# Kernel tuning notes

Measured on AMD Instinct MI355X. Metric: run time of the kernel, lower is better.

The kernel has to match this reference:

```python
import jax, jax.numpy as jnp
import numpy as np
from jax import lax

SEQ, BATCH, IN, HID, OUT = 28, 8192, 28, 128, 10


def _lstm_layer(x, W_ih, W_hh, b_ih, b_hh):
    # x: [T, B, in]; PyTorch gate order: i, f, g, o
    # precompute input projection once (keeps scan body memory-bound on h only)
    xproj = jnp.einsum('tbi,gi->tbg', x, W_ih) + b_ih + b_hh  # [T, B, 4H]
    H = W_hh.shape[1]
    B = x.shape[1]
    h0 = jnp.zeros((B, H), x.dtype)
    c0 = jnp.zeros((B, H), x.dtype)

    def step(carry, xp_t):
        h, c = carry
        gates = xp_t + h @ W_hh.T  # [B, 4H]
        i, f, g, o = jnp.split(gates, 4, axis=-1)
        i = jax.nn.sigmoid(i)
        f = jax.nn.sigmoid(f)
        g = jnp.tanh(g)
        o = jax.nn.sigmoid(o)
        c = f * c + i * g
        h = o * jnp.tanh(c)
        return (h, c), h

    _, ys = lax.scan(step, (h0, c0), xproj)
    return ys  # [T, B, H]


def setup_inputs() -> dict:
    key = jax.random.key(0)
    ks = jax.random.split(key, 11)
    s_in = 1.0 / np.sqrt(HID)
    u = lambda k, shape: jax.random.uniform(k, shape, jnp.float32, -s_in, s_in)
    return {
        'X': jax.random.normal(ks[0], (SEQ, BATCH, IN), jnp.float32),
        'W_ih0': u(ks[1], (4 * HID, IN)),
        'W_hh0': u(ks[2], (4 * HID, HID)),
        'b_ih0': u(ks[3], (4 * HID,)),
        'b_hh0': u(ks[4], (4 * HID,)),
        'W_ih1': u(ks[5], (4 * HID, HID)),
        'W_hh1': u(ks[6], (4 * HID, HID)),
        'b_ih1': u(ks[7], (4 * HID,)),
        'b_hh1': u(ks[8], (4 * HID,)),
        'W_lin': u(ks[9], (OUT, HID)),
        'b_lin': u(ks[10], (OUT,)),
    }


def reference(X, W_ih0, W_hh0, b_ih0, b_hh0, W_ih1, W_hh1, b_ih1, b_hh1, W_lin, b_lin):
    h1 = _lstm_layer(X, W_ih0, W_hh0, b_ih0, b_hh0)   # [T, B, 128]
    h2 = _lstm_layer(h1, W_ih1, W_hh1, b_ih1, b_hh1)  # [T, B, 128]
    pred = h2[-1] @ W_lin.T + b_lin                   # [B, 10]
    return pred
```

## Files before the change

kernel.cpp:

```cpp
#include <hip/hip_runtime.h>
#include <hip/hip_bf16.h>

#define SEQ   28
#define BATCH 8192
#define NIN   28
#define HID   128
#define NOUT  10

#define SCL_SIG  (-1.4426950408889634f)
#define SCL_TANH (2.8853900817779268f)

typedef __bf16 bf16_t;
typedef __bf16 bf16x8 __attribute__((ext_vector_type(8)));
typedef float  f32x4  __attribute__((ext_vector_type(4)));

__device__ __forceinline__ unsigned swz(unsigned row, unsigned byte_in_row) {
    return row * 256u + (byte_in_row ^ ((row & 7u) << 4));
}
__device__ __forceinline__ float clamp40(float x) {
    return fminf(fmaxf(x, -40.0f), 40.0f);
}

__global__ void pack_all_kernel(const float* __restrict__ X,    bf16_t* __restrict__ xpk,
                                const float* __restrict__ Whh0, bf16_t* __restrict__ whhp0,
                                const float* __restrict__ Whh1, bf16_t* __restrict__ whhp1,
                                const float* __restrict__ Wih1, bf16_t* __restrict__ wihp1) {
    const int XN = SEQ * BATCH * 32;
    const int WN = 512 * 128;
    const int total = XN + 3 * WN;
    for (int idx = blockIdx.x * blockDim.x + threadIdx.x; idx < total;
         idx += gridDim.x * blockDim.x) {
        if (idx < XN) {
            int k  = idx & 31;
            int tb = idx >> 5;
            float v = (k < NIN) ? X[(size_t)tb * NIN + k] : 0.0f;
            xpk[idx] = (bf16_t)v;
        } else {
            int r  = idx - XN;
            int mi = r / WN, e = r - mi * WN;
            const float* W = (mi == 0) ? Whh0 : (mi == 1) ? Whh1 : Wih1;
            bf16_t*      o = (mi == 0) ? whhp0 : (mi == 1) ? whhp1 : wihp1;
            int j    = e & 7;
            int frag = e >> 3;
            int lane = frag & 63;
            int ksnt = frag >> 6;
            int nt = ksnt & 31, ks = ksnt >> 5;
            int gate = nt * 16 + (lane & 15);
            int k    = ks * 32 + ((lane >> 4) << 3) + j;
            float s  = ((gate >> 7) == 2) ? SCL_TANH : SCL_SIG;
            o[e] = (bf16_t)(W[gate * 128 + k] * s);
        }
    }
}

template <int LAYER>
__global__ __launch_bounds__(512, 2)
void lstm_kernel(const float* __restrict__ Wih,
                 const float* __restrict__ bih,
                 const float* __restrict__ bhh,
                 const bf16_t* __restrict__ xin,
                 const bf16_t* __restrict__ whhp,
                 const bf16_t* __restrict__ wihp,
                 bf16_t* __restrict__ h1out,
                 const float* __restrict__ Wlin,
                 const float* __restrict__ blin,
                 float* __restrict__ out)
{
    constexpr int KS   = (LAYER == 0) ? 1 : 4;
    constexpr int XSTR = (LAYER == 0) ? 32 : 128;

    __shared__ unsigned char smem[16384] __attribute__((aligned(16)));

    const int tid  = threadIdx.x;
    const int lane = tid & 63;
    const int w    = tid >> 6;
    const int l15  = lane & 15;
    const int l4   = lane >> 4;
    const int rb   = blockIdx.x * 32;

    for (int i = tid * 16; i < 16384; i += 512 * 16) {
        f32x4 z = {0.f, 0.f, 0.f, 0.f};
        *(f32x4*)(smem + i) = z;
    }

    float bias[4];
    #pragma unroll
    for (int q = 0; q < 4; ++q) {
        int col = 16 * w + 128 * q + l15;
        float s = (q == 2) ? SCL_TANH : SCL_SIG;
        bias[q] = (bih[col] + bhh[col]) * s;
    }

    bf16x8 whh[4][4];
    #pragma unroll
    for (int q = 0; q < 4; ++q)
        #pragma unroll
        for (int ks = 0; ks < 4; ++ks)
            whh[q][ks] = *(const bf16x8*)(whhp + ((size_t)((ks * 32 + (w + 8 * q)) * 64 + lane)) * 8);

    bf16x8 wih1[4][4];
    bf16x8 wih0[4];
    if (LAYER == 1) {
        #pragma unroll
        for (int q = 0; q < 4; ++q)
            #pragma unroll
            for (int ks = 0; ks < 4; ++ks)
                wih1[q][ks] = *(const bf16x8*)(wihp + ((size_t)((ks * 32 + (w + 8 * q)) * 64 + lane)) * 8);
    } else {
        #pragma unroll
        for (int q = 0; q < 4; ++q) {
            int gate = 16 * w + 128 * q + l15;
            float s = (q == 2) ? SCL_TANH : SCL_SIG;
            #pragma unroll
            for (int j = 0; j < 8; ++j) {
                int k = l4 * 8 + j;
                wih0[q][j] = (k < NIN) ? (bf16_t)(Wih[gate * NIN + k] * s) : (bf16_t)0.0f;
            }
        }
    }

    float c[2][4] = {};

    bf16x8 x[KS][2];
    #pragma unroll
    for (int ks = 0; ks < KS; ++ks)
        #pragma unroll
        for (int m = 0; m < 2; ++m)
            x[ks][m] = *(const bf16x8*)(xin + (size_t)(rb + 16 * m + l15) * XSTR + ks * 32 + l4 * 8);

    __syncthreads();

    for (int t = 0; t < SEQ; ++t) {
        unsigned char* hb = smem + ((t & 1) << 13);
        unsigned char* hn = smem + ((~t & 1) << 13);

        bf16x8 ah[4][2];
        #pragma unroll
        for (int ks = 0; ks < 4; ++ks)
            #pragma unroll
            for (int m = 0; m < 2; ++m)
                ah[ks][m] = *(const bf16x8*)(hb + swz(16 * m + l15, (ks * 32 + l4 * 8) * 2));

        f32x4 acc[2][4];
        #pragma unroll
        for (int m = 0; m < 2; ++m)
            #pragma unroll
            for (int q = 0; q < 4; ++q) {
                f32x4 b = {bias[q], bias[q], bias[q], bias[q]};
                acc[m][q] = b;
            }

        #pragma unroll
        for (int m = 0; m < 2; ++m)
            #pragma unroll
            for (int q = 0; q < 4; ++q)
                #pragma unroll
                for (int ks = 0; ks < KS; ++ks)
                    acc[m][q] = __builtin_amdgcn_mfma_f32_16x16x32_bf16(
                        x[ks][m], (LAYER == 1) ? wih1[q][ks] : wih0[q], acc[m][q], 0, 0, 0);

        if (t + 1 < SEQ) {
            #pragma unroll
            for (int ks = 0; ks < KS; ++ks)
                #pragma unroll
                for (int m = 0; m < 2; ++m)
                    x[ks][m] = *(const bf16x8*)(xin + (size_t)((t + 1) * BATCH + rb + 16 * m + l15) * XSTR + ks * 32 + l4 * 8);
        }

        #pragma unroll
        for (int m = 0; m < 2; ++m)
            #pragma unroll
            for (int q = 0; q < 4; ++q)
                #pragma unroll
                for (int ks = 0; ks < 4; ++ks)
                    acc[m][q] = __builtin_amdgcn_mfma_f32_16x16x32_bf16(
                        ah[ks][m], whh[q][ks], acc[m][q], 0, 0, 0);

        #pragma unroll
        for (int m = 0; m < 2; ++m)
            #pragma unroll
            for (int r = 0; r < 4; ++r) {
                float Ei = __builtin_amdgcn_exp2f(clamp40(acc[m][0][r]));
                float Ef = __builtin_amdgcn_exp2f(clamp40(acc[m][1][r]));
                float Eg = __builtin_amdgcn_exp2f(clamp40(acc[m][2][r]));
                float Eo = __builtin_amdgcn_exp2f(clamp40(acc[m][3][r]));
                float ti = 1.0f + Ei, tf = 1.0f + Ef;
                float tg = 1.0f + Eg, to = 1.0f + Eo;
                float gt = 1.0f - 2.0f * __builtin_amdgcn_rcpf(tg);
                float num = fmaf(c[m][r], ti, gt * tf);
                float cn  = num * __builtin_amdgcn_rcpf(tf * ti);
                c[m][r] = cn;
                float Ec = __builtin_amdgcn_exp2f(clamp40(SCL_TANH * cn));
                float hv = (Ec - 1.0f) * __builtin_amdgcn_rcpf(to * (1.0f + Ec));
                *(bf16_t*)(hn + swz(16 * m + l4 * 4 + r, (16 * w + l15) * 2)) = (bf16_t)hv;
            }
        __syncthreads();

        if (LAYER == 0) {
            int row = tid >> 4, sc = tid & 15;
            f32x4 v = *(const f32x4*)(hn + swz(row, sc * 16));
            *(f32x4*)((unsigned char*)h1out + ((size_t)(t * BATCH + rb + row)) * 256 + sc * 16) = v;
        }
    }

    if (LAYER == 1) {
        if (tid < 32 * NOUT) {
            int row = tid / NOUT, oc = tid % NOUT;
            const unsigned char* hf = smem;
            float s = blin[oc];
            #pragma unroll 8
            for (int k = 0; k < HID; ++k) {
                float h = (float)*(const bf16_t*)(hf + swz(row, k * 2));
                s += h * Wlin[oc * HID + k];
            }
            out[(size_t)(rb + row) * NOUT + oc] = s;
        }
    }
}

extern "C" void kernel_launch(void* const* d_in, const int* in_sizes, int n_in,
                              void* d_out, int out_size, void* d_ws, size_t ws_size,
                              hipStream_t stream) {
    const float* X    = (const float*)d_in[0];
    const float* Wih0 = (const float*)d_in[1];
    const float* Whh0 = (const float*)d_in[2];
    const float* bih0 = (const float*)d_in[3];
    const float* bhh0 = (const float*)d_in[4];
    const float* Wih1 = (const float*)d_in[5];
    const float* Whh1 = (const float*)d_in[6];
    const float* bih1 = (const float*)d_in[7];
    const float* bhh1 = (const float*)d_in[8];
    const float* Wlin = (const float*)d_in[9];
    const float* blin = (const float*)d_in[10];
    float* out = (float*)d_out;

    unsigned char* ws = (unsigned char*)d_ws;
    bf16_t* xpk   = (bf16_t*)(ws);
    bf16_t* h1    = (bf16_t*)(ws + 14680064);
    bf16_t* whhp0 = (bf16_t*)(ws + 73400320);
    bf16_t* whhp1 = (bf16_t*)(ws + 73531392);
    bf16_t* wihp1 = (bf16_t*)(ws + 73662464);

    pack_all_kernel<<<dim3(4096), dim3(256), 0, stream>>>(
        X, xpk, Whh0, whhp0, Whh1, whhp1, Wih1, wihp1);

    lstm_kernel<0><<<dim3(256), dim3(512), 0, stream>>>(
        Wih0, bih0, bhh0, xpk, whhp0, (const bf16_t*)nullptr, h1,
        (const float*)nullptr, (const float*)nullptr, (float*)nullptr);

    lstm_kernel<1><<<dim3(256), dim3(512), 0, stream>>>(
        (const float*)nullptr, bih1, bhh1, h1, whhp1, wihp1, (bf16_t*)nullptr,
        Wlin, blin, out);
}
```

Measured before the change: 138.5 us.

## Fuse both LSTM layers into one kernel and convert X on the fly

Both LSTM layers now run in a single kernel: each block processes its 32 batch rows through layer 0, then reloads layer-1 weights and runs layer 1 on the h1 values it just wrote. The separate bf16 packing pass over X is removed; layer 0 reads fp32 X directly and converts it in registers. The clamps before exp2 in the gate math are also dropped. This saves a kernel launch, a large intermediate write and read, and some ALU work per step. The trade-off is a small risk of inf/NaN for extreme pre-activations, plus a longer single kernel.

```diff
diff --git a/kernel.cpp b/kernel.cpp
--- a/kernel.cpp
+++ b/kernel.cpp
@@ -17,58 +17,134 @@
 __device__ __forceinline__ unsigned swz(unsigned row, unsigned byte_in_row) {
     return row * 256u + (byte_in_row ^ ((row & 7u) << 4));
 }
-__device__ __forceinline__ float clamp40(float x) {
-    return fminf(fmaxf(x, -40.0f), 40.0f);
-}
-
-__global__ void pack_all_kernel(const float* __restrict__ X,    bf16_t* __restrict__ xpk,
-                                const float* __restrict__ Whh0, bf16_t* __restrict__ whhp0,
-                                const float* __restrict__ Whh1, bf16_t* __restrict__ whhp1,
-                                const float* __restrict__ Wih1, bf16_t* __restrict__ wihp1) {
-    const int XN = SEQ * BATCH * 32;
-    const int WN = 512 * 128;
-    const int total = XN + 3 * WN;
-    for (int idx = blockIdx.x * blockDim.x + threadIdx.x; idx < total;
-         idx += gridDim.x * blockDim.x) {
-        if (idx < XN) {
-            int k  = idx & 31;
-            int tb = idx >> 5;
-            float v = (k < NIN) ? X[(size_t)tb * NIN + k] : 0.0f;
-            xpk[idx] = (bf16_t)v;
+
+__global__ void pack_w_kernel(const float* __restrict__ Whh0, bf16_t* __restrict__ o0,
+                              const float* __restrict__ Whh1, bf16_t* __restrict__ o1,
+                              const float* __restrict__ Wih1, bf16_t* __restrict__ o2) {
+    int idx = blockIdx.x * 256 + threadIdx.x;
+    int mi = idx >> 16;
+    int e  = idx & 65535;
+    const float* W = (mi == 0) ? Whh0 : (mi == 1) ? Whh1 : Wih1;
+    bf16_t*      o = (mi == 0) ? o0   : (mi == 1) ? o1   : o2;
+    int j    = e & 7;
+    int frag = e >> 3;
+    int lane = frag & 63;
+    int ksnt = frag >> 6;
+    int nt = ksnt & 31, ks = ksnt >> 5;
+    int gate = nt * 16 + (lane & 15);
+    int k    = ks * 32 + ((lane >> 4) << 3) + j;
+    float s  = ((gate >> 7) == 2) ? SCL_TANH : SCL_SIG;
+    o[e] = (bf16_t)(W[gate * 128 + k] * s);
+}
+
+template <int LAYER>
+__device__ __forceinline__ void lstm_step(
+    int t, int rb, int tid, int lane, int w, int l15, int l4,
+    unsigned char* smem,
+    const float* __restrict__ X, const bf16_t* __restrict__ h1r,
+    bf16_t* __restrict__ h1w,
+    bf16x8 (&whh)[4][4], bf16x8 (&wih)[4][4],
+    float (&bias)[4], float (&c)[2][4], bf16x8 (&x)[4][2])
+{
+    constexpr int KS = (LAYER == 0) ? 1 : 4;
+    unsigned char* hb = smem + ((t & 1) << 13);
+    unsigned char* hn = smem + ((~t & 1) << 13);
+
+    bf16x8 ah[4][2];
+    #pragma unroll
+    for (int ks = 0; ks < 4; ++ks)
+        #pragma unroll
+        for (int m = 0; m < 2; ++m)
+            ah[ks][m] = *(const bf16x8*)(hb + swz(16 * m + l15, (ks * 32 + l4 * 8) * 2));
+
+    f32x4 acc[2][4];
+    #pragma unroll
+    for (int m = 0; m < 2; ++m)
+        #pragma unroll
+        for (int q = 0; q < 4; ++q) {
+            f32x4 b = {bias[q], bias[q], bias[q], bias[q]};
+            acc[m][q] = b;
+        }
+
+    #pragma unroll
+    for (int m = 0; m < 2; ++m)
+        #pragma unroll
+        for (int q = 0; q < 4; ++q)
+            #pragma unroll
+            for (int ks = 0; ks < KS; ++ks)
+                acc[m][q] = __builtin_amdgcn_mfma_f32_16x16x32_bf16(
+                    x[ks][m], wih[q][ks], acc[m][q], 0, 0, 0);
+
+    if (t + 1 < SEQ) {
+        if constexpr (LAYER == 0) {
+            #pragma unroll
+            for (int m = 0; m < 2; ++m) {
+                const float* base = X + ((size_t)((t + 1) * BATCH + rb + 16 * m + l15)) * NIN + l4 * 8;
+                f32x4 lo = *(const f32x4*)base;
+                f32x4 hi = {0.f, 0.f, 0.f, 0.f};
+                if (l4 < 3) hi = *(const f32x4*)(base + 4);
+                bf16x8 v;
+                #pragma unroll
+                for (int j = 0; j < 4; ++j) { v[j] = (bf16_t)lo[j]; v[4 + j] = (bf16_t)hi[j]; }
+                x[0][m] = v;
+            }
         } else {
-            int r  = idx - XN;
-            int mi = r / WN, e = r - mi * WN;
-            const float* W = (mi == 0) ? Whh0 : (mi == 1) ? Whh1 : Wih1;
-            bf16_t*      o = (mi == 0) ? whhp0 : (mi == 1) ? whhp1 : wihp1;
-            int j    = e & 7;
-            int frag = e >> 3;
-            int lane = frag & 63;
-            int ksnt = frag >> 6;
-            int nt = ksnt & 31, ks = ksnt >> 5;
-            int gate = nt * 16 + (lane & 15);
-            int k    = ks * 32 + ((lane >> 4) << 3) + j;
-            float s  = ((gate >> 7) == 2) ? SCL_TANH : SCL_SIG;
-            o[e] = (bf16_t)(W[gate * 128 + k] * s);
-        }
-    }
-}
-
-template <int LAYER>
+            #pragma unroll
+            for (int ks = 0; ks < 4; ++ks)
+                #pragma unroll
+                for (int m = 0; m < 2; ++m)
+                    x[ks][m] = *(const bf16x8*)(h1r + ((size_t)((t + 1) * BATCH + rb + 16 * m + l15)) * HID + ks * 32 + l4 * 8);
+        }
+    }
+
+    #pragma unroll
+    for (int m = 0; m < 2; ++m)
+        #pragma unroll
+        for (int q = 0; q < 4; ++q)
+            #pragma unroll
+            for (int ks = 0; ks < 4; ++ks)
+                acc[m][q] = __builtin_amdgcn_mfma_f32_16x16x32_bf16(
+                    ah[ks][m], whh[q][ks], acc[m][q], 0, 0, 0);
+
+    #pragma unroll
+    for (int m = 0; m < 2; ++m)
+        #pragma unroll
+        for (int r = 0; r < 4; ++r) {
+            float Ei = __builtin_amdgcn_exp2f(acc[m][0][r]);
+            float Ef = __builtin_amdgcn_exp2f(acc[m][1][r]);
+            float Eg = __builtin_amdgcn_exp2f(acc[m][2][r]);
+            float Eo = __builtin_amdgcn_exp2f(acc[m][3][r]);
+            float ti = 1.0f + Ei, tf = 1.0f + Ef;
+            float tg = 1.0f + Eg, to = 1.0f + Eo;
+            float gt  = fmaf(-2.0f, __builtin_amdgcn_rcpf(tg), 1.0f);
+            float rif = __builtin_amdgcn_rcpf(tf * ti);
+            float cn  = fmaf(c[m][r], ti, gt * tf) * rif;
+            c[m][r] = cn;
+            float Ec = __builtin_amdgcn_exp2f(SCL_TANH * cn);
+            float hv = (Ec - 1.0f) * __builtin_amdgcn_rcpf(to * (1.0f + Ec));
+            *(bf16_t*)(hn + swz(16 * m + l4 * 4 + r, (16 * w + l15) * 2)) = (bf16_t)hv;
+        }
+    __syncthreads();
+
+    if constexpr (LAYER == 0) {
+        int row = tid >> 4, sc = tid & 15;
+        f32x4 v = *(const f32x4*)(hn + swz(row, sc * 16));
+        *(f32x4*)((unsigned char*)h1w + ((size_t)(t * BATCH + rb + row)) * 256 + sc * 16) = v;
+    }
+}
+
 __global__ __launch_bounds__(512, 2)
-void lstm_kernel(const float* __restrict__ Wih,
-                 const float* __restrict__ bih,
-                 const float* __restrict__ bhh,
-                 const bf16_t* __restrict__ xin,
-                 const bf16_t* __restrict__ whhp,
-                 const bf16_t* __restrict__ wihp,
-                 bf16_t* __restrict__ h1out,
-                 const float* __restrict__ Wlin,
-                 const float* __restrict__ blin,
-                 float* __restrict__ out)
+void lstm_fused_kernel(const float* __restrict__ Wih0,
+                       const float* __restrict__ bih0, const float* __restrict__ bhh0,
+                       const float* __restrict__ bih1, const float* __restrict__ bhh1,
+                       const float* __restrict__ X,
+                       const bf16_t* __restrict__ whhp0,
+                       const bf16_t* __restrict__ whhp1,
+                       const bf16_t* __restrict__ wihp1,
+                       bf16_t* __restrict__ h1,
+                       const float* __restrict__ Wlin, const float* __restrict__ blin,
+                       float* __restrict__ out)
 {
-    constexpr int KS   = (LAYER == 0) ? 1 : 4;
-    constexpr int XSTR = (LAYER == 0) ? 32 : 128;
-
     __shared__ unsigned char smem[16384] __attribute__((aligned(16)));
 
     const int tid  = threadIdx.x;
@@ -78,143 +154,88 @@
     const int l4   = lane >> 4;
     const int rb   = blockIdx.x * 32;
 
+    bf16x8 whh[4][4], wih[4][4];
+    float  bias[4];
+    float  c[2][4];
+    bf16x8 x[4][2];
+
+    #pragma unroll
+    for (int q = 0; q < 4; ++q)
+        #pragma unroll
+        for (int ks = 0; ks < 4; ++ks)
+            whh[q][ks] = *(const bf16x8*)(whhp0 + ((size_t)((ks * 32 + (w + 8 * q)) * 64 + lane)) * 8);
+    #pragma unroll
+    for (int q = 0; q < 4; ++q) {
+        int gate = 16 * w + 128 * q + l15;
+        float s = (q == 2) ? SCL_TANH : SCL_SIG;
+        #pragma unroll
+        for (int j = 0; j < 8; ++j) {
+            int k = l4 * 8 + j;
+            wih[q][0][j] = (k < NIN) ? (bf16_t)(Wih0[gate * NIN + k] * s) : (bf16_t)0.0f;
+        }
+        bias[q] = (bih0[gate] + bhh0[gate]) * s;
+        c[0][q] = 0.f; c[1][q] = 0.f;
+    }
     for (int i = tid * 16; i < 16384; i += 512 * 16) {
         f32x4 z = {0.f, 0.f, 0.f, 0.f};
         *(f32x4*)(smem + i) = z;
     }
-
-    float bias[4];
+    #pragma unroll
+    for (int m = 0; m < 2; ++m) {
+        const float* base = X + ((size_t)(rb + 16 * m + l15)) * NIN + l4 * 8;
+        f32x4 lo = *(const f32x4*)base;
+        f32x4 hi = {0.f, 0.f, 0.f, 0.f};
+        if (l4 < 3) hi = *(const f32x4*)(base + 4);
+        bf16x8 v;
+        #pragma unroll
+        for (int j = 0; j < 4; ++j) { v[j] = (bf16_t)lo[j]; v[4 + j] = (bf16_t)hi[j]; }
+        x[0][m] = v;
+    }
+    __syncthreads();
+
+    for (int t = 0; t < SEQ; ++t)
+        lstm_step<0>(t, rb, tid, lane, w, l15, l4, smem, X, nullptr, h1,
+                     whh, wih, bias, c, x);
+
+    __syncthreads();
+
     #pragma unroll
     for (int q = 0; q < 4; ++q) {
-        int col = 16 * w + 128 * q + l15;
+        #pragma unroll
+        for (int ks = 0; ks < 4; ++ks) {
+            whh[q][ks] = *(const bf16x8*)(whhp1 + ((size_t)((ks * 32 + (w + 8 * q)) * 64 + lane)) * 8);
+            wih[q][ks] = *(const bf16x8*)(wihp1 + ((size_t)((ks * 32 + (w + 8 * q)) * 64 + lane)) * 8);
+        }
+        int gate = 16 * w + 128 * q + l15;
         float s = (q == 2) ? SCL_TANH : SCL_SIG;
-        bias[q] = (bih[col] + bhh[col]) * s;
-    }
-
-    bf16x8 whh[4][4];
-    #pragma unroll
-    for (int q = 0; q < 4; ++q)
-        #pragma unroll
-        for (int ks = 0; ks < 4; ++ks)
-            whh[q][ks] = *(const bf16x8*)(whhp + ((size_t)((ks * 32 + (w + 8 * q)) * 64 + lane)) * 8);
-
-    bf16x8 wih1[4][4];
-    bf16x8 wih0[4];
-    if (LAYER == 1) {
-        #pragma unroll
-        for (int q = 0; q < 4; ++q)
-            #pragma unroll
-            for (int ks = 0; ks < 4; ++ks)
-                wih1[q][ks] = *(const bf16x8*)(wihp + ((size_t)((ks * 32 + (w + 8 * q)) * 64 + lane)) * 8);
-    } else {
-        #pragma unroll
-        for (int q = 0; q < 4; ++q) {
-            int gate = 16 * w + 128 * q + l15;
-            float s = (q == 2) ? SCL_TANH : SCL_SIG;
-            #pragma unroll
-            for (int j = 0; j < 8; ++j) {
-                int k = l4 * 8 + j;
-                wih0[q][j] = (k < NIN) ? (bf16_t)(Wih[gate * NIN + k] * s) : (bf16_t)0.0f;
-            }
-        }
-    }
-
-    float c[2][4] = {};
-
-    bf16x8 x[KS][2];
-    #pragma unroll
-    for (int ks = 0; ks < KS; ++ks)
+        bias[q] = (bih1[gate] + bhh1[gate]) * s;
+        c[0][q] = 0.f; c[1][q] = 0.f;
+    }
+    for (int i = tid * 16; i < 16384; i += 512 * 16) {
+        f32x4 z = {0.f, 0.f, 0.f, 0.f};
+        *(f32x4*)(smem + i) = z;
+    }
+    #pragma unroll
+    for (int ks = 0; ks < 4; ++ks)
         #pragma unroll
         for (int m = 0; m < 2; ++m)
-            x[ks][m] = *(const bf16x8*)(xin + (size_t)(rb + 16 * m + l15) * XSTR + ks * 32 + l4 * 8);
-
-    __syncthreads();
-
-    for (int t = 0; t < SEQ; ++t) {
-        unsigned char* hb = smem + ((t & 1) << 13);
-        unsigned char* hn = smem + ((~t & 1) << 13);
-
-        bf16x8 ah[4][2];
-        #pragma unroll
-        for (int ks = 0; ks < 4; ++ks)
-            #pragma unroll
-            for (int m = 0; m < 2; ++m)
-                ah[ks][m] = *(const bf16x8*)(hb + swz(16 * m + l15, (ks * 32 + l4 * 8) * 2));
-
-        f32x4 acc[2][4];
-        #pragma unroll
-        for (int m = 0; m < 2; ++m)
-            #pragma unroll
-            for (int q = 0; q < 4; ++q) {
-                f32x4 b = {bias[q], bias[q], bias[q], bias[q]};
-                acc[m][q] = b;
-            }
-
-        #pragma unroll
-        for (int m = 0; m < 2; ++m)
-            #pragma unroll
-            for (int q = 0; q < 4; ++q)
-                #pragma unroll
-                for (int ks = 0; ks < KS; ++ks)
-                    acc[m][q] = __builtin_amdgcn_mfma_f32_16x16x32_bf16(
-                        x[ks][m], (LAYER == 1) ? wih1[q][ks] : wih0[q], acc[m][q], 0, 0, 0);
-
-        if (t + 1 < SEQ) {
-            #pragma unroll
-            for (int ks = 0; ks < KS; ++ks)
-                #pragma unroll
-                for (int m = 0; m < 2; ++m)
-                    x[ks][m] = *(const bf16x8*)(xin + (size_t)((t + 1) * BATCH + rb + 16 * m + l15) * XSTR + ks * 32 + l4 * 8);
-        }
-
-        #pragma unroll
-        for (int m = 0; m < 2; ++m)
-            #pragma unroll
-            for (int q = 0; q < 4; ++q)
-                #pragma unroll
-                for (int ks = 0; ks < 4; ++ks)
-                    acc[m][q] = __builtin_amdgcn_mfma_f32_16x16x32_bf16(
-                        ah[ks][m], whh[q][ks], acc[m][q], 0, 0, 0);
-
-        #pragma unroll
-        for (int m = 0; m < 2; ++m)
-            #pragma unroll
-            for (int r = 0; r < 4; ++r) {
-                float Ei = __builtin_amdgcn_exp2f(clamp40(acc[m][0][r]));
-                float Ef = __builtin_amdgcn_exp2f(clamp40(acc[m][1][r]));
-                float Eg = __builtin_amdgcn_exp2f(clamp40(acc[m][2][r]));
-                float Eo = __builtin_amdgcn_exp2f(clamp40(acc[m][3][r]));
-                float ti = 1.0f + Ei, tf = 1.0f + Ef;
-                float tg = 1.0f + Eg, to = 1.0f + Eo;
-                float gt = 1.0f - 2.0f * __builtin_amdgcn_rcpf(tg);
-                float num = fmaf(c[m][r], ti, gt * tf);
-                float cn  = num * __builtin_amdgcn_rcpf(tf * ti);
-                c[m][r] = cn;
-                float Ec = __builtin_amdgcn_exp2f(clamp40(SCL_TANH * cn));
-                float hv = (Ec - 1.0f) * __builtin_amdgcn_rcpf(to * (1.0f + Ec));
-                *(bf16_t*)(hn + swz(16 * m + l4 * 4 + r, (16 * w + l15) * 2)) = (bf16_t)hv;
-            }
-        __syncthreads();
-
-        if (LAYER == 0) {
-            int row = tid >> 4, sc = tid & 15;
-            f32x4 v = *(const f32x4*)(hn + swz(row, sc * 16));
-            *(f32x4*)((unsigned char*)h1out + ((size_t)(t * BATCH + rb + row)) * 256 + sc * 16) = v;
-        }
-    }
-
-    if (LAYER == 1) {
-        if (tid < 32 * NOUT) {
-            int row = tid / NOUT, oc = tid % NOUT;
-            const unsigned char* hf = smem;
-            float s = blin[oc];
-            #pragma unroll 8
-            for (int k = 0; k < HID; ++k) {
-                float h = (float)*(const bf16_t*)(hf + swz(row, k * 2));
-                s += h * Wlin[oc * HID + k];
-            }
-            out[(size_t)(rb + row) * NOUT + oc] = s;
-        }
+            x[ks][m] = *(const bf16x8*)(h1 + ((size_t)(rb + 16 * m + l15)) * HID + ks * 32 + l4 * 8);
+    __syncthreads();
+
+    for (int t = 0; t < SEQ; ++t)
+        lstm_step<1>(t, rb, tid, lane, w, l15, l4, smem, nullptr, h1, nullptr,
+                     whh, wih, bias, c, x);
+
+    if (tid < 32 * NOUT) {
+        int row = tid / NOUT, oc = tid % NOUT;
+        const unsigned char* hf = smem;
+        float s = blin[oc];
+        #pragma unroll 8
+        for (int k = 0; k < HID; ++k) {
+            float h = (float)*(const bf16_t*)(hf + swz(row, k * 2));
+            s += h * Wlin[oc * HID + k];
+        }
+        out[(size_t)(rb + row) * NOUT + oc] = s;
     }
 }
 
@@ -233,22 +254,17 @@
     const float* Wlin = (const float*)d_in[9];
     const float* blin = (const float*)d_in[10];
     float* out = (float*)d_out;
+    (void)Wih1;
 
     unsigned char* ws = (unsigned char*)d_ws;
-    bf16_t* xpk   = (bf16_t*)(ws);
-    bf16_t* h1    = (bf16_t*)(ws + 14680064);
-    bf16_t* whhp0 = (bf16_t*)(ws + 73400320);
-    bf16_t* whhp1 = (bf16_t*)(ws + 73531392);
-    bf16_t* wihp1 = (bf16_t*)(ws + 73662464);
-
-    pack_all_kernel<<<dim3(4096), dim3(256), 0, stream>>>(
-        X, xpk, Whh0, whhp0, Whh1, whhp1, Wih1, wihp1);
-
-    lstm_kernel<0><<<dim3(256), dim3(512), 0, stream>>>(
-        Wih0, bih0, bhh0, xpk, whhp0, (const bf16_t*)nullptr, h1,
-        (const float*)nullptr, (const float*)nullptr, (float*)nullptr);
-
-    lstm_kernel<1><<<dim3(256), dim3(512), 0, stream>>>(
-        (const float*)nullptr, bih1, bhh1, h1, whhp1, wihp1, (bf16_t*)nullptr,
+    bf16_t* h1    = (bf16_t*)(ws);
+    bf16_t* whhp0 = (bf16_t*)(ws + 58720256);
+    bf16_t* whhp1 = (bf16_t*)(ws + 58851328);
+    bf16_t* wihp1 = (bf16_t*)(ws + 58982400);
+
+    pack_w_kernel<<<dim3(768), dim3(256), 0, stream>>>(Whh0, whhp0, Whh1, whhp1, Wih1, wihp1);
+
+    lstm_fused_kernel<<<dim3(256), dim3(512), 0, stream>>>(
+        Wih0, bih0, bhh0, bih1, bhh1, X, whhp0, whhp1, wihp1, h1,
         Wlin, blin, out);
 }
```

After: 131.7 us. 1.05x faster.
